# Performance work log

Measured on AMD Instinct MI355X. Metric: run time of the kernel, lower is better.

## Reference

```python
import jax, jax.numpy as jnp
import numpy as np

N_NODES = 50000
N_EDGES = 1600000
D_NODE = 256
D_EDGE = 64
D_MSG = 256          # out_features_msg; each of node/edge halves is D_MSG // 2
D_OUT = 256          # out_features_reduce
H = D_MSG // 2


def setup_inputs() -> dict:
    key = jax.random.key(0)
    ks = jax.random.split(key, 10)
    x = jax.random.normal(ks[0], (N_NODES, D_NODE), dtype=jnp.float32)
    ez = jax.random.normal(ks[1], (N_EDGES, D_EDGE), dtype=jnp.float32)
    src = jax.random.randint(ks[2], (N_EDGES,), 0, N_NODES, dtype=jnp.int32)
    dst = jax.random.randint(ks[3], (N_EDGES,), 0, N_NODES, dtype=jnp.int32)
    Wn = jax.random.normal(ks[4], (H, D_NODE), dtype=jnp.float32) / np.sqrt(D_NODE)
    bn = jax.random.normal(ks[5], (H,), dtype=jnp.float32) * 0.01
    We = jax.random.normal(ks[6], (H, D_EDGE), dtype=jnp.float32) / np.sqrt(D_EDGE)
    be = jax.random.normal(ks[7], (H,), dtype=jnp.float32) * 0.01
    Wr = jax.random.normal(ks[8], (D_OUT, D_MSG), dtype=jnp.float32) / np.sqrt(D_MSG)
    br = jax.random.normal(ks[9], (D_OUT,), dtype=jnp.float32) * 0.01
    return {"x": x, "ez": ez, "src": src, "dst": dst,
            "Wn": Wn, "bn": bn, "We": We, "be": be, "Wr": Wr, "br": br}


def reference(x, ez, src, dst, Wn, bn, We, be, Wr, br):
    n = x.shape[0]
    # node/edge linear projections (message halves)
    hn = x @ Wn.T + bn                 # [N, H]
    he = ez @ We.T + be                # [E, H]
    # message for edge e is concat(hn[src[e]], he[e]); aggregate sums per dst node.
    sum_n = jax.ops.segment_sum(hn[src], dst, num_segments=n)   # [N, H]
    sum_e = jax.ops.segment_sum(he, dst, num_segments=n)        # [N, H]
    deg = jnp.zeros((n,), dtype=x.dtype).at[dst].add(1.0)       # in-degree
    # local self-state: concat(hn, zeros_H); mean over (deg + 1) states.
    denom = (deg + 1.0)[:, None]
    mean_state = jnp.concatenate([(hn + sum_n) / denom, sum_e / denom], axis=-1)  # [N, D_MSG]
    # reduce_layer is affine, so Linear(mean(states)) == mean(Linear(states)).
    out = mean_state @ Wr.T + br       # [N, D_OUT]
    # DGL degree-bucketing: zero-in-degree nodes get zero-filled output.
    out = jnp.where(deg[:, None] > 0, out, jnp.zeros((), dtype=out.dtype))
    return out
```

## Files before the change

kernel.cpp:

```cpp
#include <hip/hip_runtime.h>

#define N_NODES 50000
#define N_EDGES 1600000
#define D_NODE  256
#define D_EDGE  64
#define H       128
#define D_OUT   256

#define NPAD    50176

typedef __attribute__((ext_vector_type(8))) short bf16x8;
typedef __attribute__((ext_vector_type(4))) float f32x4;
typedef __attribute__((ext_vector_type(4))) unsigned short u16x4;

__device__ __forceinline__ float bf2f(unsigned short u) {
    union { unsigned int i; float f; } v; v.i = ((unsigned int)u) << 16; return v.f;
}
__device__ __forceinline__ unsigned short f2bf(float f) {
    union { float f; unsigned int i; } v; v.f = f;
    unsigned int r = v.i + 0x7FFFu + ((v.i >> 16) & 1u);
    return (unsigned short)(r >> 16);
}

__global__ __launch_bounds__(256) void cvt_kernel(
        const float* __restrict__ Wn, const float* __restrict__ We,
        const float* __restrict__ Wr,
        unsigned short* __restrict__ Wn_b, unsigned short* __restrict__ We_b,
        unsigned short* __restrict__ Wr_b) {
    int b = blockIdx.x;
    const float* s; unsigned short* d; int base;
    if (b < 32)      { s = Wn; d = Wn_b; base = b * 1024; }
    else if (b < 40) { s = We; d = We_b; base = (b - 32) * 1024; }
    else             { s = Wr; d = Wr_b; base = (b - 40) * 1024; }
    int i = base + threadIdx.x * 4;
    f32x4 v = *(const f32x4*)(s + i);
    u16x4 o;
    #pragma unroll
    for (int j = 0; j < 4; ++j) o[j] = f2bf(v[j]);
    *(u16x4*)(d + i) = o;
}

__global__ __launch_bounds__(64) void hn_kernel(
        const float* __restrict__ x,
        const unsigned short* __restrict__ Wn_b,
        const float* __restrict__ bn,
        unsigned short* __restrict__ hn) {
    const int lane = threadIdx.x & 63;
    const int m = lane & 15, q = lane >> 4;
    const int n0 = blockIdx.x * 16;

    f32x4 acc[8];
    #pragma unroll
    for (int t = 0; t < 8; ++t)
        #pragma unroll
        for (int r = 0; r < 4; ++r) acc[t][r] = 0.0f;

    const float* xrow = x + (size_t)(n0 + m) * D_NODE + q * 8;
    #pragma unroll
    for (int kk = 0; kk < 8; ++kk) {
        f32x4 a0 = __builtin_nontemporal_load((const f32x4*)(xrow + kk * 32));
        f32x4 a1 = __builtin_nontemporal_load((const f32x4*)(xrow + kk * 32 + 4));
        bf16x8 a;
        #pragma unroll
        for (int j = 0; j < 4; ++j) {
            a[j]     = (short)f2bf(a0[j]);
            a[4 + j] = (short)f2bf(a1[j]);
        }
        #pragma unroll
        for (int t = 0; t < 8; ++t) {
            bf16x8 b = *(const bf16x8*)(Wn_b + (size_t)(t * 16 + m) * D_NODE + kk * 32 + q * 8);
            acc[t] = __builtin_amdgcn_mfma_f32_16x16x32_bf16(a, b, acc[t], 0, 0, 0);
        }
    }
    #pragma unroll
    for (int t = 0; t < 8; ++t) {
        int o = t * 16 + m;
        float bv = bn[o];
        #pragma unroll
        for (int r = 0; r < 4; ++r) {
            int node = n0 + q * 4 + r;
            hn[(size_t)node * H + o] = f2bf(acc[t][r] + bv);
        }
    }
}

__global__ __launch_bounds__(256) void hist_kernel(
        const int* __restrict__ dst, unsigned int* __restrict__ cnt) {
    int e = blockIdx.x * 256 + threadIdx.x;
    atomicAdd(&cnt[dst[e]], 1u);
}

__device__ __forceinline__ unsigned int block_scan_incl(unsigned int v, unsigned int* wtot) {
    const int lane = threadIdx.x & 63;
    const int wid = threadIdx.x >> 6;
    unsigned int x = v;
    #pragma unroll
    for (int off = 1; off < 64; off <<= 1) {
        unsigned int y = __shfl_up(x, off, 64);
        if (lane >= off) x += y;
    }
    if (lane == 63) wtot[wid] = x;
    __syncthreads();
    unsigned int wof = 0;
    #pragma unroll
    for (int w = 0; w < 4; ++w) if (w < wid) wof += wtot[w];
    return x + wof;
}

__global__ __launch_bounds__(256) void scan1_kernel(
        const unsigned int* __restrict__ cnt,
        unsigned int* __restrict__ partial,
        unsigned int* __restrict__ blocksum) {
    __shared__ unsigned int wtot[4];
    int i = blockIdx.x * 256 + threadIdx.x;
    unsigned int v = cnt[i];
    unsigned int inc = block_scan_incl(v, wtot);
    partial[i] = inc - v;
    if (threadIdx.x == 255) blocksum[blockIdx.x] = inc;
}

__global__ __launch_bounds__(256) void scan2_kernel(
        const unsigned int* __restrict__ blocksum,
        unsigned int* __restrict__ blockoff) {
    __shared__ unsigned int wtot[4];
    unsigned int v = blocksum[threadIdx.x];
    unsigned int inc = block_scan_incl(v, wtot);
    blockoff[threadIdx.x] = inc - v;
}

__global__ __launch_bounds__(256) void scatter_kernel(
        const int* __restrict__ src, const int* __restrict__ dst,
        unsigned int* __restrict__ partial,
        const unsigned int* __restrict__ blockoff,
        unsigned long long* __restrict__ eid_src) {
    int e = blockIdx.x * 256 + threadIdx.x;
    int d = dst[e];
    unsigned int s = (unsigned int)src[e];
    unsigned int pos = atomicAdd(&partial[d], 1u) + blockoff[d >> 8];
    eid_src[pos] = ((unsigned long long)s << 32) | (unsigned int)e;
}

__global__ __launch_bounds__(256) void fused_kernel(
        const unsigned long long* __restrict__ eid_src,
        const unsigned int* __restrict__ partial,
        const unsigned int* __restrict__ blockoff,
        const unsigned int* __restrict__ cnt,
        const float* __restrict__ ez,
        const unsigned int* __restrict__ hn32,
        const unsigned short* __restrict__ We_b,
        const float* __restrict__ be,
        const unsigned short* __restrict__ Wr_b,
        const float* __restrict__ br,
        float* __restrict__ out) {
    __shared__ __align__(16) unsigned short ms[16][264];
    __shared__ __align__(16) float seL[16][68];
    __shared__ float rden[16];
    __shared__ float degf[16];

    const int t = threadIdx.x;
    const int n0 = blockIdx.x * 16;
    const int wid = t >> 6;
    const int lane = t & 63;

    if (t < 16) {
        unsigned int dg = cnt[n0 + t];
        degf[t] = (float)dg;
        rden[t] = 1.0f / (1.0f + (float)dg);
    }

    for (int nl = 0; nl < 4; ++nl) {
        const int row = wid * 4 + nl;
        const int n = n0 + row;
        const unsigned int c = cnt[n];
        const unsigned int end = partial[n] + blockoff[n >> 8];
        const unsigned int beg = end - c;
        float se = 0.0f, sn0 = 0.0f, sn1 = 0.0f;

        for (unsigned int base = beg; base < end; base += 64) {
            int mcnt = (int)(end - base); if (mcnt > 64) mcnt = 64;
            unsigned long long ent = (lane < mcnt)
                ? __builtin_nontemporal_load(eid_src + base + lane) : 0ULL;
            unsigned int elo = (unsigned int)ent;
            unsigned int shi = (unsigned int)(ent >> 32);

            int j = 0;
            for (; j + 8 <= mcnt; j += 8) {
                unsigned int e[8], s[8];
                #pragma unroll
                for (int u = 0; u < 8; ++u) {
                    e[u] = __shfl(elo, j + u, 64);
                    s[u] = __shfl(shi, j + u, 64);
                }
                float a[8]; unsigned int h[8];
                #pragma unroll
                for (int u = 0; u < 8; ++u)
                    a[u] = __builtin_nontemporal_load(ez + (size_t)e[u] * D_EDGE + lane);
                #pragma unroll
                for (int u = 0; u < 8; ++u)
                    h[u] = hn32[(size_t)s[u] * 64 + lane];
                #pragma unroll
                for (int u = 0; u < 8; ++u) {
                    se += a[u];
                    union { unsigned int ui; float f; } lo, hi;
                    lo.ui = h[u] << 16; hi.ui = h[u] & 0xffff0000u;
                    sn0 += lo.f; sn1 += hi.f;
                }
            }
            for (; j < mcnt; ++j) {
                unsigned int e0 = __shfl(elo, j, 64), s0 = __shfl(shi, j, 64);
                float a0 = __builtin_nontemporal_load(ez + (size_t)e0 * D_EDGE + lane);
                unsigned int h0 = hn32[(size_t)s0 * 64 + lane];
                se += a0;
                union { unsigned int ui; float f; } lo, hi;
                lo.ui = h0 << 16; hi.ui = h0 & 0xffff0000u;
                sn0 += lo.f; sn1 += hi.f;
            }
        }

        seL[row][lane] = se;
        unsigned int hv = hn32[(size_t)n * 64 + lane];
        float rd = 1.0f / (1.0f + (float)c);
        union { unsigned int ui; float f; } lo, hi;
        lo.ui = hv << 16; hi.ui = hv & 0xffff0000u;
        unsigned int p = ((unsigned int)f2bf((hi.f + sn1) * rd) << 16)
                       |  (unsigned int)f2bf((lo.f + sn0) * rd);
        *(unsigned int*)&ms[row][2 * lane] = p;
    }
    __syncthreads();

    {
        const int m = lane & 15, q = lane >> 4;
        f32x4 acc[2];
        #pragma unroll
        for (int i = 0; i < 2; ++i)
            #pragma unroll
            for (int r = 0; r < 4; ++r) acc[i][r] = 0.0f;

        #pragma unroll
        for (int kk = 0; kk < 2; ++kk) {
            const float* ap = &seL[m][kk * 32 + q * 8];
            f32x4 a0 = *(const f32x4*)ap;
            f32x4 a1 = *(const f32x4*)(ap + 4);
            bf16x8 a;
            #pragma unroll
            for (int j = 0; j < 4; ++j) {
                a[j]     = (short)f2bf(a0[j]);
                a[4 + j] = (short)f2bf(a1[j]);
            }
            #pragma unroll
            for (int i = 0; i < 2; ++i) {
                int o0 = (wid + 4 * i) * 16;
                bf16x8 b = *(const bf16x8*)(We_b + (size_t)(o0 + m) * D_EDGE + kk * 32 + q * 8);
                acc[i] = __builtin_amdgcn_mfma_f32_16x16x32_bf16(a, b, acc[i], 0, 0, 0);
            }
        }
        #pragma unroll
        for (int i = 0; i < 2; ++i) {
            int o = (wid + 4 * i) * 16 + m;
            float bev = be[o];
            #pragma unroll
            for (int r = 0; r < 4; ++r) {
                int nl = q * 4 + r;
                float val = (acc[i][r] + degf[nl] * bev) * rden[nl];
                ms[nl][128 + o] = f2bf(val);
            }
        }
    }
    __syncthreads();

    {
        const int m = lane & 15, q = lane >> 4;
        f32x4 acc[4];
        #pragma unroll
        for (int i = 0; i < 4; ++i)
            #pragma unroll
            for (int r = 0; r < 4; ++r) acc[i][r] = 0.0f;

        #pragma unroll
        for (int kk = 0; kk < 8; ++kk) {
            bf16x8 a = *(const bf16x8*)&ms[m][kk * 32 + q * 8];
            #pragma unroll
            for (int i = 0; i < 4; ++i) {
                int o0 = (wid * 4 + i) * 16;
                bf16x8 b = *(const bf16x8*)(Wr_b + (size_t)(o0 + m) * 256 + kk * 32 + q * 8);
                acc[i] = __builtin_amdgcn_mfma_f32_16x16x32_bf16(a, b, acc[i], 0, 0, 0);
            }
        }
        #pragma unroll
        for (int i = 0; i < 4; ++i) {
            int o = (wid * 4 + i) * 16 + m;
            float brv = br[o];
            #pragma unroll
            for (int r = 0; r < 4; ++r) {
                int nl = q * 4 + r;
                float val = acc[i][r] + brv;
                if (degf[nl] == 0.0f) val = 0.0f;
                __builtin_nontemporal_store(val, out + (size_t)(n0 + nl) * D_OUT + o);
            }
        }
    }
}

extern "C" void kernel_launch(void* const* d_in, const int* in_sizes, int n_in,
                              void* d_out, int out_size, void* d_ws, size_t ws_size,
                              hipStream_t stream) {
    const float* x  = (const float*)d_in[0];
    const float* ez = (const float*)d_in[1];
    const int* src  = (const int*)d_in[2];
    const int* dst  = (const int*)d_in[3];
    const float* Wn = (const float*)d_in[4];
    const float* bn = (const float*)d_in[5];
    const float* We = (const float*)d_in[6];
    const float* be = (const float*)d_in[7];
    const float* Wr = (const float*)d_in[8];
    const float* br = (const float*)d_in[9];
    float* out      = (float*)d_out;

    unsigned int* cnt      = (unsigned int*)d_ws;
    unsigned int* blocksum = cnt + NPAD;
    unsigned int* blockoff = blocksum + 256;
    unsigned int* partial  = blockoff + 256;
    unsigned long long* eid_src = (unsigned long long*)(partial + NPAD);
    unsigned short* hn = (unsigned short*)(eid_src + N_EDGES);
    unsigned short* Wn_b = hn + (size_t)N_NODES * H;
    unsigned short* We_b = Wn_b + 32768;
    unsigned short* Wr_b = We_b + 8192;

    hipMemsetAsync(d_ws, 0, (size_t)(NPAD + 256) * 4, stream);

    cvt_kernel<<<104, 256, 0, stream>>>(Wn, We, Wr, Wn_b, We_b, Wr_b);
    hn_kernel<<<N_NODES / 16, 64, 0, stream>>>(x, Wn_b, bn, hn);
    hist_kernel<<<N_EDGES / 256, 256, 0, stream>>>(dst, cnt);
    scan1_kernel<<<NPAD / 256, 256, 0, stream>>>(cnt, partial, blocksum);
    scan2_kernel<<<1, 256, 0, stream>>>(blocksum, blockoff);
    scatter_kernel<<<N_EDGES / 256, 256, 0, stream>>>(src, dst, partial, blockoff, eid_src);
    fused_kernel<<<N_NODES / 16, 256, 0, stream>>>(eid_src, partial, blockoff, cnt, ez,
                                                   (const unsigned int*)hn,
                                                   We_b, be, Wr_b, br, out);
}
```

Measured before the change: 872.6 us.

## Merge hn GEMM with histogram, vectorize scatter and gather loads

```diff
diff --git a/kernel.cpp b/kernel.cpp
--- a/kernel.cpp
+++ b/kernel.cpp
@@ -9,9 +9,15 @@
 
 #define NPAD    50176
 
+#define HN_TILES   3125
+#define HN_BLOCKS  782
+#define E4_BLOCKS  1563
+
 typedef __attribute__((ext_vector_type(8))) short bf16x8;
 typedef __attribute__((ext_vector_type(4))) float f32x4;
 typedef __attribute__((ext_vector_type(4))) unsigned short u16x4;
+typedef __attribute__((ext_vector_type(4))) unsigned int u32x4;
+typedef __attribute__((ext_vector_type(4))) int i32x4;
 
 __device__ __forceinline__ float bf2f(unsigned short u) {
     union { unsigned int i; float f; } v; v.i = ((unsigned int)u) << 16; return v.f;
@@ -40,54 +46,66 @@
     *(u16x4*)(d + i) = o;
 }
 
-__global__ __launch_bounds__(64) void hn_kernel(
+__global__ __launch_bounds__(256) void front_kernel(
         const float* __restrict__ x,
         const unsigned short* __restrict__ Wn_b,
         const float* __restrict__ bn,
-        unsigned short* __restrict__ hn) {
-    const int lane = threadIdx.x & 63;
-    const int m = lane & 15, q = lane >> 4;
-    const int n0 = blockIdx.x * 16;
-
-    f32x4 acc[8];
-    #pragma unroll
-    for (int t = 0; t < 8; ++t)
-        #pragma unroll
-        for (int r = 0; r < 4; ++r) acc[t][r] = 0.0f;
-
-    const float* xrow = x + (size_t)(n0 + m) * D_NODE + q * 8;
-    #pragma unroll
-    for (int kk = 0; kk < 8; ++kk) {
-        f32x4 a0 = __builtin_nontemporal_load((const f32x4*)(xrow + kk * 32));
-        f32x4 a1 = __builtin_nontemporal_load((const f32x4*)(xrow + kk * 32 + 4));
-        bf16x8 a;
-        #pragma unroll
-        for (int j = 0; j < 4; ++j) {
-            a[j]     = (short)f2bf(a0[j]);
-            a[4 + j] = (short)f2bf(a1[j]);
+        unsigned short* __restrict__ hn,
+        const int* __restrict__ dst,
+        unsigned int* __restrict__ cnt) {
+    const int b = blockIdx.x;
+    if (b < HN_BLOCKS) {
+        const int wid = threadIdx.x >> 6;
+        const int lane = threadIdx.x & 63;
+        const int tile = b * 4 + wid;
+        if (tile >= HN_TILES) return;
+        const int m = lane & 15, q = lane >> 4;
+        const int n0 = tile * 16;
+
+        f32x4 acc[8];
+        #pragma unroll
+        for (int t = 0; t < 8; ++t)
+            #pragma unroll
+            for (int r = 0; r < 4; ++r) acc[t][r] = 0.0f;
+
+        const float* xrow = x + (size_t)(n0 + m) * D_NODE + q * 8;
+        #pragma unroll
+        for (int kk = 0; kk < 8; ++kk) {
+            f32x4 a0 = __builtin_nontemporal_load((const f32x4*)(xrow + kk * 32));
+            f32x4 a1 = __builtin_nontemporal_load((const f32x4*)(xrow + kk * 32 + 4));
+            bf16x8 a;
+            #pragma unroll
+            for (int j = 0; j < 4; ++j) {
+                a[j]     = (short)f2bf(a0[j]);
+                a[4 + j] = (short)f2bf(a1[j]);
+            }
+            #pragma unroll
+            for (int t = 0; t < 8; ++t) {
+                bf16x8 bb = *(const bf16x8*)(Wn_b + (size_t)(t * 16 + m) * D_NODE + kk * 32 + q * 8);
+                acc[t] = __builtin_amdgcn_mfma_f32_16x16x32_bf16(a, bb, acc[t], 0, 0, 0);
+            }
         }
         #pragma unroll
         for (int t = 0; t < 8; ++t) {
-            bf16x8 b = *(const bf16x8*)(Wn_b + (size_t)(t * 16 + m) * D_NODE + kk * 32 + q * 8);
-            acc[t] = __builtin_amdgcn_mfma_f32_16x16x32_bf16(a, b, acc[t], 0, 0, 0);
-        }
-    }
-    #pragma unroll
-    for (int t = 0; t < 8; ++t) {
-        int o = t * 16 + m;
-        float bv = bn[o];
-        #pragma unroll
-        for (int r = 0; r < 4; ++r) {
-            int node = n0 + q * 4 + r;
-            hn[(size_t)node * H + o] = f2bf(acc[t][r] + bv);
-        }
-    }
-}
-
-__global__ __launch_bounds__(256) void hist_kernel(
-        const int* __restrict__ dst, unsigned int* __restrict__ cnt) {
-    int e = blockIdx.x * 256 + threadIdx.x;
-    atomicAdd(&cnt[dst[e]], 1u);
+            int o = t * 16 + m;
+            float bv = bn[o];
+            #pragma unroll
+            for (int r = 0; r < 4; ++r) {
+                int node = n0 + q * 4 + r;
+                hn[(size_t)node * H + o] = f2bf(acc[t][r] + bv);
+            }
+        }
+    } else {
+        const int idx = (b - HN_BLOCKS) * 256 + threadIdx.x;
+        const int e0 = idx * 4;
+        if (e0 < N_EDGES) {
+            i32x4 d4 = *(const i32x4*)(dst + e0);
+            atomicAdd(&cnt[d4[0]], 1u);
+            atomicAdd(&cnt[d4[1]], 1u);
+            atomicAdd(&cnt[d4[2]], 1u);
+            atomicAdd(&cnt[d4[3]], 1u);
+        }
+    }
 }
 
 __device__ __forceinline__ unsigned int block_scan_incl(unsigned int v, unsigned int* wtot) {
@@ -133,11 +151,17 @@
         unsigned int* __restrict__ partial,
         const unsigned int* __restrict__ blockoff,
         unsigned long long* __restrict__ eid_src) {
-    int e = blockIdx.x * 256 + threadIdx.x;
-    int d = dst[e];
-    unsigned int s = (unsigned int)src[e];
-    unsigned int pos = atomicAdd(&partial[d], 1u) + blockoff[d >> 8];
-    eid_src[pos] = ((unsigned long long)s << 32) | (unsigned int)e;
+    const int idx = blockIdx.x * 256 + threadIdx.x;
+    const int e0 = idx * 4;
+    if (e0 >= N_EDGES) return;
+    i32x4 s4 = *(const i32x4*)(src + e0);
+    i32x4 d4 = *(const i32x4*)(dst + e0);
+    #pragma unroll
+    for (int k = 0; k < 4; ++k) {
+        int d = d4[k];
+        unsigned int pos = atomicAdd(&partial[d], 1u) + blockoff[d >> 8];
+        eid_src[pos] = ((unsigned long long)(unsigned int)s4[k] << 32) | (unsigned int)(e0 + k);
+    }
 }
 
 __global__ __launch_bounds__(256) void fused_kernel(
@@ -161,6 +185,8 @@
     const int n0 = blockIdx.x * 16;
     const int wid = t >> 6;
     const int lane = t & 63;
+    const int q = lane >> 4;
+    const int l16 = lane & 15;
 
     if (t < 16) {
         unsigned int dg = cnt[n0 + t];
@@ -174,7 +200,10 @@
         const unsigned int c = cnt[n];
         const unsigned int end = partial[n] + blockoff[n >> 8];
         const unsigned int beg = end - c;
-        float se = 0.0f, sn0 = 0.0f, sn1 = 0.0f;
+
+        f32x4 sez; sez[0] = sez[1] = sez[2] = sez[3] = 0.0f;
+        float snlo[4] = {0.f, 0.f, 0.f, 0.f};
+        float snhi[4] = {0.f, 0.f, 0.f, 0.f};
 
         for (unsigned int base = beg; base < end; base += 64) {
             int mcnt = (int)(end - base); if (mcnt > 64) mcnt = 64;
@@ -185,51 +214,71 @@
 
             int j = 0;
             for (; j + 8 <= mcnt; j += 8) {
-                unsigned int e[8], s[8];
+                unsigned int e0 = __shfl(elo, j + q, 64);
+                unsigned int s0 = __shfl(shi, j + q, 64);
+                unsigned int e1 = __shfl(elo, j + 4 + q, 64);
+                unsigned int s1 = __shfl(shi, j + 4 + q, 64);
+                f32x4 a0 = __builtin_nontemporal_load((const f32x4*)(ez + (size_t)e0 * D_EDGE + l16 * 4));
+                f32x4 a1 = __builtin_nontemporal_load((const f32x4*)(ez + (size_t)e1 * D_EDGE + l16 * 4));
+                u32x4 h0 = *(const u32x4*)(hn32 + (size_t)s0 * 64 + l16 * 4);
+                u32x4 h1 = *(const u32x4*)(hn32 + (size_t)s1 * 64 + l16 * 4);
+                sez += a0; sez += a1;
                 #pragma unroll
-                for (int u = 0; u < 8; ++u) {
-                    e[u] = __shfl(elo, j + u, 64);
-                    s[u] = __shfl(shi, j + u, 64);
+                for (int k = 0; k < 4; ++k) {
+                    union { unsigned int ui; float f; } lo, hi;
+                    lo.ui = h0[k] << 16; hi.ui = h0[k] & 0xffff0000u;
+                    snlo[k] += lo.f; snhi[k] += hi.f;
+                    lo.ui = h1[k] << 16; hi.ui = h1[k] & 0xffff0000u;
+                    snlo[k] += lo.f; snhi[k] += hi.f;
                 }
-                float a[8]; unsigned int h[8];
-                #pragma unroll
-                for (int u = 0; u < 8; ++u)
-                    a[u] = __builtin_nontemporal_load(ez + (size_t)e[u] * D_EDGE + lane);
-                #pragma unroll
-                for (int u = 0; u < 8; ++u)
-                    h[u] = hn32[(size_t)s[u] * 64 + lane];
-                #pragma unroll
-                for (int u = 0; u < 8; ++u) {
-                    se += a[u];
-                    union { unsigned int ui; float f; } lo, hi;
-                    lo.ui = h[u] << 16; hi.ui = h[u] & 0xffff0000u;
-                    sn0 += lo.f; sn1 += hi.f;
+            }
+            for (; j < mcnt; j += 4) {
+                int i0 = j + q;
+                unsigned int e0 = __shfl(elo, i0, 64);
+                unsigned int s0 = __shfl(shi, i0, 64);
+                if (i0 < mcnt) {
+                    f32x4 a0 = __builtin_nontemporal_load((const f32x4*)(ez + (size_t)e0 * D_EDGE + l16 * 4));
+                    u32x4 h0 = *(const u32x4*)(hn32 + (size_t)s0 * 64 + l16 * 4);
+                    sez += a0;
+                    #pragma unroll
+                    for (int k = 0; k < 4; ++k) {
+                        union { unsigned int ui; float f; } lo, hi;
+                        lo.ui = h0[k] << 16; hi.ui = h0[k] & 0xffff0000u;
+                        snlo[k] += lo.f; snhi[k] += hi.f;
+                    }
                 }
             }
-            for (; j < mcnt; ++j) {
-                unsigned int e0 = __shfl(elo, j, 64), s0 = __shfl(shi, j, 64);
-                float a0 = __builtin_nontemporal_load(ez + (size_t)e0 * D_EDGE + lane);
-                unsigned int h0 = hn32[(size_t)s0 * 64 + lane];
-                se += a0;
+        }
+
+        #pragma unroll
+        for (int k = 0; k < 4; ++k) {
+            sez[k]  += __shfl_xor(sez[k], 16, 64);
+            sez[k]  += __shfl_xor(sez[k], 32, 64);
+            snlo[k] += __shfl_xor(snlo[k], 16, 64);
+            snlo[k] += __shfl_xor(snlo[k], 32, 64);
+            snhi[k] += __shfl_xor(snhi[k], 16, 64);
+            snhi[k] += __shfl_xor(snhi[k], 32, 64);
+        }
+
+        if (q == 0) {
+            float rd = 1.0f / (1.0f + (float)c);
+            *(f32x4*)&seL[row][l16 * 4] = sez;
+            u32x4 hv = *(const u32x4*)(hn32 + (size_t)n * 64 + l16 * 4);
+            u32x4 pk;
+            #pragma unroll
+            for (int k = 0; k < 4; ++k) {
                 union { unsigned int ui; float f; } lo, hi;
-                lo.ui = h0 << 16; hi.ui = h0 & 0xffff0000u;
-                sn0 += lo.f; sn1 += hi.f;
-            }
-        }
-
-        seL[row][lane] = se;
-        unsigned int hv = hn32[(size_t)n * 64 + lane];
-        float rd = 1.0f / (1.0f + (float)c);
-        union { unsigned int ui; float f; } lo, hi;
-        lo.ui = hv << 16; hi.ui = hv & 0xffff0000u;
-        unsigned int p = ((unsigned int)f2bf((hi.f + sn1) * rd) << 16)
-                       |  (unsigned int)f2bf((lo.f + sn0) * rd);
-        *(unsigned int*)&ms[row][2 * lane] = p;
+                lo.ui = hv[k] << 16; hi.ui = hv[k] & 0xffff0000u;
+                pk[k] = ((unsigned int)f2bf((hi.f + snhi[k]) * rd) << 16)
+                      |  (unsigned int)f2bf((lo.f + snlo[k]) * rd);
+            }
+            *(u32x4*)&ms[row][l16 * 8] = pk;
+        }
     }
     __syncthreads();
 
     {
-        const int m = lane & 15, q = lane >> 4;
+        const int m = lane & 15, qq = lane >> 4;
         f32x4 acc[2];
         #pragma unroll
         for (int i = 0; i < 2; ++i)
@@ -238,7 +287,7 @@
 
         #pragma unroll
         for (int kk = 0; kk < 2; ++kk) {
-            const float* ap = &seL[m][kk * 32 + q * 8];
+            const float* ap = &seL[m][kk * 32 + qq * 8];
             f32x4 a0 = *(const f32x4*)ap;
             f32x4 a1 = *(const f32x4*)(ap + 4);
             bf16x8 a;
@@ -250,7 +299,7 @@
             #pragma unroll
             for (int i = 0; i < 2; ++i) {
                 int o0 = (wid + 4 * i) * 16;
-                bf16x8 b = *(const bf16x8*)(We_b + (size_t)(o0 + m) * D_EDGE + kk * 32 + q * 8);
+                bf16x8 b = *(const bf16x8*)(We_b + (size_t)(o0 + m) * D_EDGE + kk * 32 + qq * 8);
                 acc[i] = __builtin_amdgcn_mfma_f32_16x16x32_bf16(a, b, acc[i], 0, 0, 0);
             }
         }
@@ -260,7 +309,7 @@
             float bev = be[o];
             #pragma unroll
             for (int r = 0; r < 4; ++r) {
-                int nl = q * 4 + r;
+                int nl = qq * 4 + r;
                 float val = (acc[i][r] + degf[nl] * bev) * rden[nl];
                 ms[nl][128 + o] = f2bf(val);
             }
@@ -269,7 +318,7 @@
     __syncthreads();
 
     {
-        const int m = lane & 15, q = lane >> 4;
+        const int m = lane & 15, qq = lane >> 4;
         f32x4 acc[4];
         #pragma unroll
         for (int i = 0; i < 4; ++i)
@@ -278,11 +327,11 @@
 
         #pragma unroll
         for (int kk = 0; kk < 8; ++kk) {
-            bf16x8 a = *(const bf16x8*)&ms[m][kk * 32 + q * 8];
+            bf16x8 a = *(const bf16x8*)&ms[m][kk * 32 + qq * 8];
             #pragma unroll
             for (int i = 0; i < 4; ++i) {
                 int o0 = (wid * 4 + i) * 16;
-                bf16x8 b = *(const bf16x8*)(Wr_b + (size_t)(o0 + m) * 256 + kk * 32 + q * 8);
+                bf16x8 b = *(const bf16x8*)(Wr_b + (size_t)(o0 + m) * 256 + kk * 32 + qq * 8);
                 acc[i] = __builtin_amdgcn_mfma_f32_16x16x32_bf16(a, b, acc[i], 0, 0, 0);
             }
         }
@@ -292,7 +341,7 @@
             float brv = br[o];
             #pragma unroll
             for (int r = 0; r < 4; ++r) {
-                int nl = q * 4 + r;
+                int nl = qq * 4 + r;
                 float val = acc[i][r] + brv;
                 if (degf[nl] == 0.0f) val = 0.0f;
                 __builtin_nontemporal_store(val, out + (size_t)(n0 + nl) * D_OUT + o);
@@ -329,11 +378,10 @@
     hipMemsetAsync(d_ws, 0, (size_t)(NPAD + 256) * 4, stream);
 
     cvt_kernel<<<104, 256, 0, stream>>>(Wn, We, Wr, Wn_b, We_b, Wr_b);
-    hn_kernel<<<N_NODES / 16, 64, 0, stream>>>(x, Wn_b, bn, hn);
-    hist_kernel<<<N_EDGES / 256, 256, 0, stream>>>(dst, cnt);
+    front_kernel<<<HN_BLOCKS + E4_BLOCKS, 256, 0, stream>>>(x, Wn_b, bn, hn, dst, cnt);
     scan1_kernel<<<NPAD / 256, 256, 0, stream>>>(cnt, partial, blocksum);
     scan2_kernel<<<1, 256, 0, stream>>>(blocksum, blockoff);
-    scatter_kernel<<<N_EDGES / 256, 256, 0, stream>>>(src, dst, partial, blockoff, eid_src);
+    scatter_kernel<<<E4_BLOCKS, 256, 0, stream>>>(src, dst, partial, blockoff, eid_src);
     fused_kernel<<<N_NODES / 16, 256, 0, stream>>>(eid_src, partial, blockoff, cnt, ez,
                                                    (const unsigned int*)hn,
                                                    We_b, be, Wr_b, br, out);
```

New measurement: 846.4 us. -3.0%, faster.
